# Kernel optimization log

Hardware: AMD Instinct MI355X
Metric: run time of the kernel (lower is better)

The kernel has to match this reference:

```python
import jax, jax.numpy as jnp
import numpy as np

B, T, I, H = 256, 512, 300, 128


def setup_inputs() -> dict:
    key = jax.random.key(0)
    ks = jax.random.split(key, 7)
    s_ih = 1.0 / np.sqrt(H)
    return {
        "x": jax.random.normal(ks[0], (B, T, I), dtype=jnp.float32),
        # PyTorch LSTM params, gate order i,f,g,o stacked along first axis
        "W_ih": jax.random.uniform(ks[1], (4 * H, I), minval=-s_ih, maxval=s_ih, dtype=jnp.float32),
        "W_hh": jax.random.uniform(ks[2], (4 * H, H), minval=-s_ih, maxval=s_ih, dtype=jnp.float32),
        "b_ih": jax.random.uniform(ks[3], (4 * H,), minval=-s_ih, maxval=s_ih, dtype=jnp.float32),
        "b_hh": jax.random.uniform(ks[4], (4 * H,), minval=-s_ih, maxval=s_ih, dtype=jnp.float32),
        "fc_w": jax.random.uniform(ks[5], (1, H), minval=-s_ih, maxval=s_ih, dtype=jnp.float32),
        "fc_b": jax.random.uniform(ks[6], (1,), minval=-s_ih, maxval=s_ih, dtype=jnp.float32),
    }


def _lstm_last_h(x, W_ih, W_hh, b_ih, b_hh):
    # Precompute input contributions for all timesteps at once: [B,T,4H]
    xg = jnp.einsum("bti,gi->btg", x, W_ih) + b_ih + b_hh
    xg = jnp.transpose(xg, (1, 0, 2))  # [T,B,4H] for scan

    def step(carry, xg_t):
        h, c = carry
        gates = xg_t + h @ W_hh.T  # [B,4H]
        i, f, g, o = jnp.split(gates, 4, axis=-1)
        i = jax.nn.sigmoid(i)
        f = jax.nn.sigmoid(f)
        g = jnp.tanh(g)
        o = jax.nn.sigmoid(o)
        c = f * c + i * g
        h = o * jnp.tanh(c)
        return (h, c), None

    h0 = jnp.zeros((x.shape[0], W_hh.shape[1]), dtype=x.dtype)
    (h_last, _), _ = jax.lax.scan(step, (h0, h0), xg)
    return h_last  # [B,H]


def reference(x, W_ih, W_hh, b_ih, b_hh, fc_w, fc_b):
    h_last = _lstm_last_h(x, W_ih, W_hh, b_ih, b_hh)
    return h_last @ fc_w.T + fc_b  # [B,1]
```

## Files before the change

kernel.cpp:

```cpp
#include <hip/hip_runtime.h>
#include <cstdint>
#include <cstddef>

#define Bb   256
#define Tt   512
#define Ii   300
#define Hh   128
#define G4   512
#define KP   320

typedef _Float16 h2v   __attribute__((ext_vector_type(2)));
typedef _Float16 half8 __attribute__((ext_vector_type(8)));
typedef float    f32x4 __attribute__((ext_vector_type(4)));

typedef __attribute__((address_space(3))) unsigned int lds_uint;
typedef const __attribute__((address_space(1))) unsigned int glb_uint;

static __device__ __forceinline__ h2v as_h2(unsigned int u){ union{unsigned int u; h2v h;} c; c.u=u; return c.h; }
static __device__ __forceinline__ unsigned int as_u32(h2v h){ union{unsigned int u; h2v h;} c; c.h=h; return c.u; }

#if __has_builtin(__builtin_amdgcn_fdot2)
#define FDOT2(a,b,c) __builtin_amdgcn_fdot2((a),(b),(c),false)
#else
static __device__ __forceinline__ float FDOT2(h2v a, h2v b, float c){
  return c + (float)a[0]*(float)b[0] + (float)a[1]*(float)b[1];
}
#endif

__global__ __launch_bounds__(256) void conv_x(const float* __restrict__ x, unsigned int* __restrict__ x16){
  int idx = blockIdx.x*256 + threadIdx.x;
  int r   = idx / 160;
  int kk2 = idx - r*160;
  int kk  = kk2*2;
  const float* xr = x + (size_t)r*Ii;
  float v0 = (kk   < Ii) ? xr[kk]   : 0.f;
  float v1 = (kk+1 < Ii) ? xr[kk+1] : 0.f;
  h2v h; h[0] = (_Float16)v0; h[1] = (_Float16)v1;
  x16[idx] = as_u32(h);
}

__global__ __launch_bounds__(256) void conv_small(const float* __restrict__ Wih, const float* __restrict__ Whh,
      const float* __restrict__ bih, const float* __restrict__ bhh,
      unsigned int* __restrict__ W16, unsigned int* __restrict__ Whh2, float* __restrict__ bias){
  int idx = blockIdx.x*256 + threadIdx.x;
  if (idx < G4*160){
    int r = idx/160, kk2 = idx - r*160, kk = kk2*2;
    const float* wr = Wih + (size_t)r*Ii;
    float v0 = (kk   < Ii) ? wr[kk]   : 0.f;
    float v1 = (kk+1 < Ii) ? wr[kk+1] : 0.f;
    h2v h; h[0]=(_Float16)v0; h[1]=(_Float16)v1;
    W16[idx] = as_u32(h);
  } else if (idx < G4*160 + G4*64){
    int t = idx - G4*160; int j = t>>6, kk = t&63;
    float v0 = Whh[j*Hh + kk*2], v1 = Whh[j*Hh + kk*2 + 1];
    h2v h; h[0]=(_Float16)v0; h[1]=(_Float16)v1;
    Whh2[t] = as_u32(h);
  } else if (idx < G4*160 + G4*64 + G4){
    int d = idx - (G4*160 + G4*64);
    bias[d] = bih[d] + bhh[d];
  }
}

__global__ __launch_bounds__(256,2) void gemm16(const _Float16* __restrict__ A, const _Float16* __restrict__ Bm,
       const float* __restrict__ bias, float* __restrict__ C){
  __shared__ __align__(16) _Float16 As[128*32];
  __shared__ __align__(16) _Float16 Bs[128*32];
  int tid = threadIdx.x;
  int w = tid>>6, lane = tid&63;
  int bm = blockIdx.x*128, bn = blockIdx.y*128;
  f32x4 acc[2][8];
  #pragma unroll
  for (int i=0;i<2;i++)
    #pragma unroll
    for (int j=0;j<8;j++) acc[i][j] = (f32x4){0.f,0.f,0.f,0.f};

  int L0 = w*128 + lane, L1 = L0 + 64;
  int r0 = L0>>2, c0 = (L0&3) ^ (r0&3);
  int r1 = L1>>2, c1 = (L1&3) ^ (r1&3);
  const _Float16* gA0 = A  + (size_t)(bm+r0)*KP + c0*8;
  const _Float16* gA1 = A  + (size_t)(bm+r1)*KP + c1*8;
  const _Float16* gB0 = Bm + (size_t)(bn+r0)*KP + c0*8;
  const _Float16* gB1 = Bm + (size_t)(bn+r1)*KP + c1*8;

  int q = lane>>4, mr = lane&15;
  int m0 = w*32;
  int ra0 = m0+mr, ra1 = m0+16+mr;
  int oa0 = ra0*32 + ((q ^ (ra0&3))*8);
  int oa1 = ra1*32 + ((q ^ (ra1&3))*8);
  int ob[8];
  #pragma unroll
  for (int j=0;j<8;j++){ int rb = j*16+mr; ob[j] = rb*32 + ((q ^ (rb&3))*8); }

  for (int kt=0; kt<KP/32; ++kt){
    __syncthreads();
    __builtin_amdgcn_global_load_lds((glb_uint*)gA0, (lds_uint*)&As[w*1024      ], 16, 0, 0);
    __builtin_amdgcn_global_load_lds((glb_uint*)gA1, (lds_uint*)&As[w*1024 + 512], 16, 0, 0);
    __builtin_amdgcn_global_load_lds((glb_uint*)gB0, (lds_uint*)&Bs[w*1024      ], 16, 0, 0);
    __builtin_amdgcn_global_load_lds((glb_uint*)gB1, (lds_uint*)&Bs[w*1024 + 512], 16, 0, 0);
    gA0 += 32; gA1 += 32; gB0 += 32; gB1 += 32;
    __syncthreads();
    half8 af0 = *(const half8*)&As[oa0];
    half8 af1 = *(const half8*)&As[oa1];
    #pragma unroll
    for (int j=0;j<8;j++){
      half8 bf = *(const half8*)&Bs[ob[j]];
      acc[0][j] = __builtin_amdgcn_mfma_f32_16x16x32_f16(af0, bf, acc[0][j], 0,0,0);
      acc[1][j] = __builtin_amdgcn_mfma_f32_16x16x32_f16(af1, bf, acc[1][j], 0,0,0);
    }
  }
  #pragma unroll
  for (int j=0;j<8;j++){
    int gc = bn + j*16 + mr;
    float bv = bias[gc];
    #pragma unroll
    for (int i=0;i<2;i++){
      int gr0 = bm + w*32 + i*16 + q*4;
      #pragma unroll
      for (int reg=0; reg<4; ++reg)
        C[(size_t)(gr0+reg)*G4 + gc] = acc[i][j][reg] + bv;
    }
  }
}

__global__ __launch_bounds__(1024,4) void lstm_rec(const float* __restrict__ xg, const unsigned int* __restrict__ Whh2,
     const float* __restrict__ fcw, const float* __restrict__ fcb, float* __restrict__ out){
  int tid = threadIdx.x;
  int b = blockIdx.x;
  int r = tid >> 1;
  int s = tid & 1;
  int d = r & 127;
  h2v w[32];
  #pragma unroll
  for (int k=0; k<32; ++k) w[k] = as_h2(Whh2[r*64 + s*32 + k]);

  __shared__ __align__(16) unsigned short hsh[128];
  __shared__ float gsh[512];
  __shared__ float red[128];
  if (tid < 128) hsh[tid] = 0;
  float creg = 0.f, hreg = 0.f;
  const float* xrow = xg + (size_t)b * (Tt*G4);
  float xc = xrow[r];
  __syncthreads();

  for (int t=0; t<Tt; ++t){
    float xn = 0.f;
    if (t < Tt-1) xn = xrow[(size_t)(t+1)*G4 + r];
    float a0 = (s==0) ? xc : 0.f, a1 = 0.f;
    const uint4* hv = ((const uint4*)hsh) + s*8;
    #pragma unroll
    for (int kq=0; kq<8; ++kq){
      uint4 hq = hv[kq];
      a0 = FDOT2(as_h2(hq.x), w[kq*4+0], a0);
      a1 = FDOT2(as_h2(hq.y), w[kq*4+1], a1);
      a0 = FDOT2(as_h2(hq.z), w[kq*4+2], a0);
      a1 = FDOT2(as_h2(hq.w), w[kq*4+3], a1);
    }
    float a = a0 + a1;
    a += __shfl_xor(a, 1, 64);
    float act;
    if ((r >> 7) == 2){ float e = __expf(2.f*a); act = 1.f - 2.f/(e+1.f); }
    else              { act = 1.f/(1.f+__expf(-a)); }
    if (s == 0) gsh[r] = act;
    __syncthreads();
    float gi = gsh[d], gf = gsh[128+d], gg = gsh[256+d], go = gsh[384+d];
    creg = gf*creg + gi*gg;
    float ec = __expf(2.f*creg); float tc = 1.f - 2.f/(ec+1.f);
    hreg = go*tc;
    if (tid < 256 && s == 0){
      union{ _Float16 f; unsigned short u; } cv; cv.f = (_Float16)hreg;
      hsh[r] = cv.u;
    }
    __syncthreads();
    xc = xn;
  }

  if (tid < 256 && s == 0) red[r] = hreg * fcw[r];
  __syncthreads();
  #pragma unroll
  for (int st=64; st>=1; st>>=1){
    if (tid < st) red[tid] += red[tid+st];
    __syncthreads();
  }
  if (tid == 0) out[b] = red[0] + fcb[0];
}

extern "C" void kernel_launch(void* const* d_in, const int* in_sizes, int n_in,
                              void* d_out, int out_size, void* d_ws, size_t ws_size,
                              hipStream_t stream){
  const float* x   = (const float*)d_in[0];
  const float* Wih = (const float*)d_in[1];
  const float* Whh = (const float*)d_in[2];
  const float* bih = (const float*)d_in[3];
  const float* bhh = (const float*)d_in[4];
  const float* fcw = (const float*)d_in[5];
  const float* fcb = (const float*)d_in[6];
  float* out = (float*)d_out;
  char* ws = (char*)d_ws;

  unsigned int* x16   = (unsigned int*)(ws);
  unsigned int* W16   = (unsigned int*)(ws + 83886080);
  unsigned int* Whh2w = (unsigned int*)(ws + 84213760);
  float*        bias  = (float*)      (ws + 84344832);
  float*        xg    = (float*)      (ws + 84346880);

  hipLaunchKernelGGL(conv_x,     dim3(81920),  dim3(256), 0, stream, x, x16);
  hipLaunchKernelGGL(conv_small, dim3(450),    dim3(256), 0, stream, Wih, Whh, bih, bhh, W16, Whh2w, bias);
  hipLaunchKernelGGL(gemm16,     dim3(1024,4), dim3(256), 0, stream,
                     (const _Float16*)x16, (const _Float16*)W16, bias, xg);
  hipLaunchKernelGGL(lstm_rec,   dim3(256),    dim3(1024), 0, stream, xg, Whh2w, fcw, fcb, out);
}
```

Measured before the change: 732.4 us.

## Compute recurrent h·W_hh with MFMA using a single-row A operand

Replaces the per-thread fdot2 recurrent matvec (1024 threads, two threads per gate row) with MFMA 16x16x32 instructions on 8 waves of 512 threads. The h vector is loaded into row 0 of the A operand and the other 15 rows are zeroed, so 15/16 of the MFMA work is wasted. Gate activations and the cell update are now done by 128 threads, with the input projection added after the matmul, and the final FC reduction uses wave shuffles instead of an LDS tree. The goal is to cut per-step instruction count and block size on the serial recurrence. The cost is padding waste in the MFMA and the MFMA latency chain sitting on the critical path of every timestep.

```diff
diff --git a/kernel.cpp b/kernel.cpp
--- a/kernel.cpp
+++ b/kernel.cpp
@@ -18,14 +18,7 @@
 
 static __device__ __forceinline__ h2v as_h2(unsigned int u){ union{unsigned int u; h2v h;} c; c.u=u; return c.h; }
 static __device__ __forceinline__ unsigned int as_u32(h2v h){ union{unsigned int u; h2v h;} c; c.h=h; return c.u; }
-
-#if __has_builtin(__builtin_amdgcn_fdot2)
-#define FDOT2(a,b,c) __builtin_amdgcn_fdot2((a),(b),(c),false)
-#else
-static __device__ __forceinline__ float FDOT2(h2v a, h2v b, float c){
-  return c + (float)a[0]*(float)b[0] + (float)a[1]*(float)b[1];
-}
-#endif
+static __device__ __forceinline__ half8 as_half8(uint4 u){ union{uint4 u; half8 h;} c; c.u=u; return c.h; }
 
 __global__ __launch_bounds__(256) void conv_x(const float* __restrict__ x, unsigned int* __restrict__ x16){
   int idx = blockIdx.x*256 + threadIdx.x;
@@ -122,66 +115,88 @@
   }
 }
 
-__global__ __launch_bounds__(1024,4) void lstm_rec(const float* __restrict__ xg, const unsigned int* __restrict__ Whh2,
+__global__ __launch_bounds__(512,2) void lstm_rec(const float* __restrict__ xg, const unsigned int* __restrict__ Whh2,
      const float* __restrict__ fcw, const float* __restrict__ fcb, float* __restrict__ out){
   int tid = threadIdx.x;
   int b = blockIdx.x;
-  int r = tid >> 1;
-  int s = tid & 1;
-  int d = r & 127;
-  h2v w[32];
-  #pragma unroll
-  for (int k=0; k<32; ++k) w[k] = as_h2(Whh2[r*64 + s*32 + k]);
-
-  __shared__ __align__(16) unsigned short hsh[128];
+  int w = tid>>6, lane = tid&63;
+  int q = lane>>4, mr = lane&15;
+  int nb = w*64;
+
+  uint4 bf[4][4];
+  #pragma unroll
+  for (int jn=0; jn<4; ++jn)
+    #pragma unroll
+    for (int kt=0; kt<4; ++kt)
+      bf[jn][kt] = *(const uint4*)&Whh2[(size_t)(nb + jn*16 + mr)*64 + kt*16 + q*4];
+
+  __shared__ __align__(16) _Float16 hA[128];
   __shared__ float gsh[512];
-  __shared__ float red[128];
-  if (tid < 128) hsh[tid] = 0;
+  __shared__ float red[8];
+  if (tid < 64) ((unsigned int*)hA)[tid] = 0;
+
+  bool act = (lane < 16);
+  int d = nb/4 + mr;
+  const float* xrow = xg + (size_t)b * (Tt*G4);
+  float xc0=0.f, xc1=0.f, xc2=0.f, xc3=0.f;
+  if (act){ xc0 = xrow[d]; xc1 = xrow[128+d]; xc2 = xrow[256+d]; xc3 = xrow[384+d]; }
   float creg = 0.f, hreg = 0.f;
-  const float* xrow = xg + (size_t)b * (Tt*G4);
-  float xc = xrow[r];
   __syncthreads();
 
   for (int t=0; t<Tt; ++t){
-    float xn = 0.f;
-    if (t < Tt-1) xn = xrow[(size_t)(t+1)*G4 + r];
-    float a0 = (s==0) ? xc : 0.f, a1 = 0.f;
-    const uint4* hv = ((const uint4*)hsh) + s*8;
-    #pragma unroll
-    for (int kq=0; kq<8; ++kq){
-      uint4 hq = hv[kq];
-      a0 = FDOT2(as_h2(hq.x), w[kq*4+0], a0);
-      a1 = FDOT2(as_h2(hq.y), w[kq*4+1], a1);
-      a0 = FDOT2(as_h2(hq.z), w[kq*4+2], a0);
-      a1 = FDOT2(as_h2(hq.w), w[kq*4+3], a1);
-    }
-    float a = a0 + a1;
-    a += __shfl_xor(a, 1, 64);
-    float act;
-    if ((r >> 7) == 2){ float e = __expf(2.f*a); act = 1.f - 2.f/(e+1.f); }
-    else              { act = 1.f/(1.f+__expf(-a)); }
-    if (s == 0) gsh[r] = act;
-    __syncthreads();
-    float gi = gsh[d], gf = gsh[128+d], gg = gsh[256+d], go = gsh[384+d];
-    creg = gf*creg + gi*gg;
-    float ec = __expf(2.f*creg); float tc = 1.f - 2.f/(ec+1.f);
-    hreg = go*tc;
-    if (tid < 256 && s == 0){
-      union{ _Float16 f; unsigned short u; } cv; cv.f = (_Float16)hreg;
-      hsh[r] = cv.u;
-    }
-    __syncthreads();
-    xc = xn;
-  }
-
-  if (tid < 256 && s == 0) red[r] = hreg * fcw[r];
+    float xn0=0.f, xn1=0.f, xn2=0.f, xn3=0.f;
+    {
+      int tn = (t+1 < Tt) ? t+1 : t;
+      const float* xr = xrow + (size_t)tn*G4;
+      if (act){ xn0 = xr[d]; xn1 = xr[128+d]; xn2 = xr[256+d]; xn3 = xr[384+d]; }
+    }
+    half8 a[4];
+    #pragma unroll
+    for (int kt=0; kt<4; ++kt){
+      half8 v = (half8){0,0,0,0,0,0,0,0};
+      if (mr == 0) v = *(const half8*)&hA[kt*32 + q*8];
+      a[kt] = v;
+    }
+    #pragma unroll
+    for (int jn=0; jn<4; ++jn){
+      f32x4 acc = (f32x4){0.f,0.f,0.f,0.f};
+      #pragma unroll
+      for (int kt=0; kt<4; ++kt)
+        acc = __builtin_amdgcn_mfma_f32_16x16x32_f16(a[kt], as_half8(bf[jn][kt]), acc, 0,0,0);
+      if (q == 0) gsh[nb + jn*16 + mr] = acc[0];
+    }
+    __syncthreads();
+    if (act){
+      float ai = gsh[      d] + xc0;
+      float af = gsh[128 + d] + xc1;
+      float ag = gsh[256 + d] + xc2;
+      float ao = gsh[384 + d] + xc3;
+      float i_ = 1.f/(1.f+__expf(-ai));
+      float f_ = 1.f/(1.f+__expf(-af));
+      float eg = __expf(2.f*ag); float g_ = 1.f - 2.f/(eg+1.f);
+      float o_ = 1.f/(1.f+__expf(-ao));
+      creg = f_*creg + i_*g_;
+      float ec = __expf(2.f*creg); float tc = 1.f - 2.f/(ec+1.f);
+      hreg = o_*tc;
+      hA[d] = (_Float16)hreg;
+      xc0 = xn0; xc1 = xn1; xc2 = xn2; xc3 = xn3;
+    }
+    __syncthreads();
+  }
+
+  float p = act ? hreg * fcw[d] : 0.f;
+  p += __shfl_xor(p, 1, 64);
+  p += __shfl_xor(p, 2, 64);
+  p += __shfl_xor(p, 4, 64);
+  p += __shfl_xor(p, 8, 64);
+  if (lane == 0) red[w] = p;
   __syncthreads();
-  #pragma unroll
-  for (int st=64; st>=1; st>>=1){
-    if (tid < st) red[tid] += red[tid+st];
-    __syncthreads();
-  }
-  if (tid == 0) out[b] = red[0] + fcb[0];
+  if (tid == 0){
+    float s = fcb[0];
+    #pragma unroll
+    for (int k=0;k<8;k++) s += red[k];
+    out[b] = s;
+  }
 }
 
 extern "C" void kernel_launch(void* const* d_in, const int* in_sizes, int n_in,
@@ -207,5 +222,5 @@
   hipLaunchKernelGGL(conv_small, dim3(450),    dim3(256), 0, stream, Wih, Whh, bih, bhh, W16, Whh2w, bias);
   hipLaunchKernelGGL(gemm16,     dim3(1024,4), dim3(256), 0, stream,
                      (const _Float16*)x16, (const _Float16*)W16, bias, xg);
-  hipLaunchKernelGGL(lstm_rec,   dim3(256),    dim3(1024), 0, stream, xg, Whh2w, fcw, fcb, out);
-}
+  hipLaunchKernelGGL(lstm_rec,   dim3(256),    dim3(512), 0, stream, xg, Whh2w, fcw, fcb, out);
+}
```

Measured after the change: 939.1 us. +28.2%, slower.

## Halve recurrent block size and double-buffer xg chunks into LDS

Applied to the files above, without the earlier changes.

The recurrent LSTM kernel now uses 512 threads, one per gate row holding all 64 packed W_hh pairs in registers, so the cross-lane shuffle reduction is gone. The per-timestep global load of the precomputed input gates is replaced by async global-to-LDS staging of 16-timestep chunks, double-buffered. The final FC reduction uses wave shuffles instead of an LDS tree. The cost is higher register pressure per thread and 64KB of LDS per block. The second buffer is refilled after only one barrier with no explicit wait on the async loads, so correctness relies on the per-timestep barriers draining them.

```diff
diff --git a/kernel.cpp b/kernel.cpp
--- a/kernel.cpp
+++ b/kernel.cpp
@@ -122,66 +122,79 @@
   }
 }
 
-__global__ __launch_bounds__(1024,4) void lstm_rec(const float* __restrict__ xg, const unsigned int* __restrict__ Whh2,
+__global__ __launch_bounds__(512,2) void lstm_rec(const float* __restrict__ xg, const unsigned int* __restrict__ Whh2,
      const float* __restrict__ fcw, const float* __restrict__ fcb, float* __restrict__ out){
   int tid = threadIdx.x;
   int b = blockIdx.x;
-  int r = tid >> 1;
-  int s = tid & 1;
-  int d = r & 127;
-  h2v w[32];
-  #pragma unroll
-  for (int k=0; k<32; ++k) w[k] = as_h2(Whh2[r*64 + s*32 + k]);
+  int d = tid & 127;
+  h2v w[64];
+  #pragma unroll
+  for (int k=0; k<64; ++k) w[k] = as_h2(Whh2[tid*64 + k]);
 
   __shared__ __align__(16) unsigned short hsh[128];
   __shared__ float gsh[512];
-  __shared__ float red[128];
-  if (tid < 128) hsh[tid] = 0;
+  __shared__ __align__(16) float xbuf[2][16*G4];
+  if (tid < 64) ((unsigned int*)hsh)[tid] = 0;
+
+  const float* xrow = xg + (size_t)b * (Tt*G4);
+  int wv = tid >> 6, lane = tid & 63;
+
+  auto stage = [&](int c){
+    const float* src = xrow + (size_t)c*16*G4;
+    float* dst = xbuf[c & 1];
+    #pragma unroll
+    for (int i=0; i<4; ++i){
+      int off = i*2048 + wv*256;
+      __builtin_amdgcn_global_load_lds((glb_uint*)(src + off + lane*4),
+                                       (lds_uint*)(dst + off), 16, 0, 0);
+    }
+  };
+
+  stage(0);
   float creg = 0.f, hreg = 0.f;
-  const float* xrow = xg + (size_t)b * (Tt*G4);
-  float xc = xrow[r];
   __syncthreads();
 
   for (int t=0; t<Tt; ++t){
-    float xn = 0.f;
-    if (t < Tt-1) xn = xrow[(size_t)(t+1)*G4 + r];
-    float a0 = (s==0) ? xc : 0.f, a1 = 0.f;
-    const uint4* hv = ((const uint4*)hsh) + s*8;
+    if ((t & 15) == 0){
+      int nc = (t >> 4) + 1;
+      if (nc < Tt/16) stage(nc);
+    }
+    float xv = xbuf[(t >> 4) & 1][(t & 15)*G4 + tid];
+    float a0 = 0.f, a1 = 0.f;
+    const uint4* hv = (const uint4*)hsh;
     #pragma unroll
     for (int kq=0; kq<8; ++kq){
-      uint4 hq = hv[kq];
-      a0 = FDOT2(as_h2(hq.x), w[kq*4+0], a0);
-      a1 = FDOT2(as_h2(hq.y), w[kq*4+1], a1);
-      a0 = FDOT2(as_h2(hq.z), w[kq*4+2], a0);
-      a1 = FDOT2(as_h2(hq.w), w[kq*4+3], a1);
-    }
-    float a = a0 + a1;
-    a += __shfl_xor(a, 1, 64);
+      uint4 hq0 = hv[kq*2], hq1 = hv[kq*2+1];
+      a0 = FDOT2(as_h2(hq0.x), w[kq*8+0], a0); a1 = FDOT2(as_h2(hq0.y), w[kq*8+1], a1);
+      a0 = FDOT2(as_h2(hq0.z), w[kq*8+2], a0); a1 = FDOT2(as_h2(hq0.w), w[kq*8+3], a1);
+      a0 = FDOT2(as_h2(hq1.x), w[kq*8+4], a0); a1 = FDOT2(as_h2(hq1.y), w[kq*8+5], a1);
+      a0 = FDOT2(as_h2(hq1.z), w[kq*8+6], a0); a1 = FDOT2(as_h2(hq1.w), w[kq*8+7], a1);
+    }
+    float a = a0 + a1 + xv;
     float act;
-    if ((r >> 7) == 2){ float e = __expf(2.f*a); act = 1.f - 2.f/(e+1.f); }
-    else              { act = 1.f/(1.f+__expf(-a)); }
-    if (s == 0) gsh[r] = act;
+    if ((tid >> 7) == 2){ float e = __expf(2.f*a); act = 1.f - 2.f/(e+1.f); }
+    else                { act = 1.f/(1.f+__expf(-a)); }
+    gsh[tid] = act;
     __syncthreads();
     float gi = gsh[d], gf = gsh[128+d], gg = gsh[256+d], go = gsh[384+d];
     creg = gf*creg + gi*gg;
     float ec = __expf(2.f*creg); float tc = 1.f - 2.f/(ec+1.f);
     hreg = go*tc;
-    if (tid < 256 && s == 0){
+    if (tid < 128){
       union{ _Float16 f; unsigned short u; } cv; cv.f = (_Float16)hreg;
-      hsh[r] = cv.u;
-    }
-    __syncthreads();
-    xc = xn;
-  }
-
-  if (tid < 256 && s == 0) red[r] = hreg * fcw[r];
+      hsh[tid] = cv.u;
+    }
+    __syncthreads();
+  }
+
+  if (tid < 128) gsh[tid] = hreg * fcw[tid];
   __syncthreads();
-  #pragma unroll
-  for (int st=64; st>=1; st>>=1){
-    if (tid < st) red[tid] += red[tid+st];
-    __syncthreads();
-  }
-  if (tid == 0) out[b] = red[0] + fcb[0];
+  if (tid < 64){
+    float s = gsh[tid] + gsh[tid+64];
+    #pragma unroll
+    for (int st=32; st>=1; st>>=1) s += __shfl_down(s, st, 64);
+    if (tid == 0) out[b] = s + fcb[0];
+  }
 }
 
 extern "C" void kernel_launch(void* const* d_in, const int* in_sizes, int n_in,
@@ -207,5 +220,5 @@
   hipLaunchKernelGGL(conv_small, dim3(450),    dim3(256), 0, stream, Wih, Whh, bih, bhh, W16, Whh2w, bias);
   hipLaunchKernelGGL(gemm16,     dim3(1024,4), dim3(256), 0, stream,
                      (const _Float16*)x16, (const _Float16*)W16, bias, xg);
-  hipLaunchKernelGGL(lstm_rec,   dim3(256),    dim3(1024), 0, stream, xg, Whh2w, fcw, fcb, out);
-}
+  hipLaunchKernelGGL(lstm_rec,   dim3(256),    dim3(512), 0, stream, xg, Whh2w, fcw, fcb, out);
+}
```

New measurement: 723.7 us. Within noise of the previous version (-1.2%).
